# Kernel optimization log

Hardware: AMD Instinct MI355X
Metric: run time of the kernel (lower is better)

## Reference

```python
import jax, jax.numpy as jnp
import numpy as np


def setup_inputs() -> dict:
    key = jax.random.key(0)
    ks = jax.random.split(key, 6)
    B, N, F = 32, 2048, 64
    C1, C2, H = 32, 32, 512
    x = jax.random.normal(ks[0], (B, N, F), dtype=jnp.float32)
    a = jax.random.uniform(ks[1], (B, N, N), dtype=jnp.float32)
    W1 = jax.random.normal(ks[2], (F, C1), dtype=jnp.float32) * (1.0 / np.sqrt(F))
    b1 = jnp.zeros((C1,), dtype=jnp.float32)
    W2 = jax.random.normal(ks[3], (C1, C2), dtype=jnp.float32) * (1.0 / np.sqrt(C1))
    b2 = jnp.zeros((C2,), dtype=jnp.float32)
    Wf1 = jax.random.normal(ks[4], (C2, H), dtype=jnp.float32) * (1.0 / np.sqrt(C2))
    bf1 = jnp.zeros((H,), dtype=jnp.float32)
    Wf2 = jax.random.normal(ks[5], (H, 1), dtype=jnp.float32) * (1.0 / np.sqrt(H))
    bf2 = jnp.zeros((1,), dtype=jnp.float32)
    return {"x": x, "a": a, "W1": W1, "b1": b1, "W2": W2, "b2": b2,
            "Wf1": Wf1, "bf1": bf1, "Wf2": Wf2, "bf2": bf2}


def _gcn(x, a, W, b):
    # GCNConv batch mode: act(A @ X @ W + b); project first (cheaper: F -> C)
    xw = jnp.einsum('bnf,fc->bnc', x, W)
    return jax.nn.relu(jnp.einsum('bnm,bmc->bnc', a, xw) + b)


def reference(x, a, W1, b1, W2, b2, Wf1, bf1, Wf2, bf2):
    h = _gcn(x, a, W1, b1)          # [B,N,32]
    h = _gcn(h, a, W2, b2)          # [B,N,32]
    pooled = jnp.sum(h, axis=1)     # GlobalSumPool over nodes -> [B,32]
    h = jax.nn.relu(pooled @ Wf1 + bf1)  # [B,512]
    out = h @ Wf2 + bf2             # linear output activation -> [B,1]
    return out
```

## Files before the change

### kernel.cpp

```cpp
#include <hip/hip_runtime.h>

using bf16x8 = __attribute__((ext_vector_type(8))) short;
using f32x4  = __attribute__((ext_vector_type(4))) float;

static constexpr int NN = 2048;
static constexpr int NB = 32;
static constexpr int NC = 32;

__device__ __forceinline__ unsigned short f2bf(float f) {
    unsigned int u = __float_as_uint(f);
    u += 0x7FFFu + ((u >> 16) & 1u);
    return (unsigned short)(u >> 16);
}

template<int INCH>
__global__ void proj_kernel(const float* __restrict__ X, const float* __restrict__ W,
                            unsigned short* __restrict__ XWt)
{
    __shared__ float wlds[INCH * NC];
    const int b = blockIdx.y;
    const int m = blockIdx.x * 256 + threadIdx.x;
    for (int i = threadIdx.x; i < INCH * NC; i += 256) wlds[i] = W[i];
    __syncthreads();

    const float* xrow = X + ((size_t)b * NN + m) * INCH;
    float acc[NC];
#pragma unroll
    for (int c = 0; c < NC; ++c) acc[c] = 0.f;

    for (int f = 0; f < INCH; f += 4) {
        const float4 v = *reinterpret_cast<const float4*>(xrow + f);
        const float xv[4] = {v.x, v.y, v.z, v.w};
#pragma unroll
        for (int j = 0; j < 4; ++j) {
#pragma unroll
            for (int c = 0; c < NC; ++c)
                acc[c] += xv[j] * wlds[(f + j) * NC + c];
        }
    }

    unsigned short* outp = XWt + (size_t)b * NC * NN + m;
#pragma unroll
    for (int c = 0; c < NC; ++c) outp[(size_t)c * NN] = f2bf(acc[c]);
}

template<bool WRITE_H>
__global__ void gcn_gemm(const float* __restrict__ A, const unsigned short* __restrict__ Bt,
                         const float* __restrict__ bias, float* __restrict__ Hout,
                         float* __restrict__ pooled)
{
    const int b    = blockIdx.y;
    const int wave = threadIdx.x >> 6;
    const int lane = threadIdx.x & 63;
    const int lr   = lane & 15;
    const int kg   = lane >> 4;

    const int r0 = blockIdx.x * 64 + wave * 16;

    const float*          ap  = A  + ((size_t)b * NN + (r0 + lr)) * NN + kg * 8;
    const unsigned short* bp0 = Bt + ((size_t)b * NC + lr) * NN + kg * 8;
    const unsigned short* bp1 = bp0 + (size_t)16 * NN;

    f32x4 acc0 = {0.f, 0.f, 0.f, 0.f};
    f32x4 acc1 = {0.f, 0.f, 0.f, 0.f};

    for (int k = 0; k < NN; k += 128) {
        float4 xa[8];
        bf16x8 bb0[4], bb1[4];
#pragma unroll
        for (int s = 0; s < 4; ++s) {
            xa[2 * s]     = *reinterpret_cast<const float4*>(ap + s * 32);
            xa[2 * s + 1] = *reinterpret_cast<const float4*>(ap + s * 32 + 4);
            bb0[s] = *reinterpret_cast<const bf16x8*>(bp0 + s * 32);
            bb1[s] = *reinterpret_cast<const bf16x8*>(bp1 + s * 32);
        }
        ap += 128; bp0 += 128; bp1 += 128;

#pragma unroll
        for (int s = 0; s < 4; ++s) {
            bf16x8 af;
            af[0] = (short)f2bf(xa[2 * s].x); af[1] = (short)f2bf(xa[2 * s].y);
            af[2] = (short)f2bf(xa[2 * s].z); af[3] = (short)f2bf(xa[2 * s].w);
            af[4] = (short)f2bf(xa[2 * s + 1].x); af[5] = (short)f2bf(xa[2 * s + 1].y);
            af[6] = (short)f2bf(xa[2 * s + 1].z); af[7] = (short)f2bf(xa[2 * s + 1].w);

            acc0 = __builtin_amdgcn_mfma_f32_16x16x32_bf16(af, bb0[s], acc0, 0, 0, 0);
            acc1 = __builtin_amdgcn_mfma_f32_16x16x32_bf16(af, bb1[s], acc1, 0, 0, 0);
        }
    }

    const float bias0 = bias[lr];
    const float bias1 = bias[lr + 16];

    if constexpr (WRITE_H) {
#pragma unroll
        for (int j = 0; j < 4; ++j) {
            const int row = r0 + kg * 4 + j;
            float* hp = Hout + ((size_t)b * NN + row) * NC;
            hp[lr]      = fmaxf(acc0[j] + bias0, 0.f);
            hp[lr + 16] = fmaxf(acc1[j] + bias1, 0.f);
        }
    } else {
        float s0 = 0.f, s1 = 0.f;
#pragma unroll
        for (int j = 0; j < 4; ++j) {
            s0 += fmaxf(acc0[j] + bias0, 0.f);
            s1 += fmaxf(acc1[j] + bias1, 0.f);
        }
        s0 += __shfl_xor(s0, 16); s0 += __shfl_xor(s0, 32);
        s1 += __shfl_xor(s1, 16); s1 += __shfl_xor(s1, 32);
        if (kg == 0) {
            atomicAdd(&pooled[b * NC + lr],      s0);
            atomicAdd(&pooled[b * NC + 16 + lr], s1);
        }
    }
}

__global__ void head_kernel(const float* __restrict__ pooled,
                            const float* __restrict__ Wf1, const float* __restrict__ bf1,
                            const float* __restrict__ Wf2, const float* __restrict__ bf2,
                            float* __restrict__ out)
{
    const int b = blockIdx.x;
    const int h = threadIdx.x;

    float dot = 0.f;
#pragma unroll
    for (int c = 0; c < NC; ++c)
        dot += pooled[b * NC + c] * Wf1[c * 512 + h];

    const float v   = fmaxf(dot + bf1[h], 0.f);
    float part      = v * Wf2[h];

#pragma unroll
    for (int off = 32; off >= 1; off >>= 1)
        part += __shfl_xor(part, off);

    __shared__ float red[8];
    if ((threadIdx.x & 63) == 0) red[threadIdx.x >> 6] = part;
    __syncthreads();
    if (threadIdx.x == 0) {
        float s = 0.f;
#pragma unroll
        for (int i = 0; i < 8; ++i) s += red[i];
        out[b] = s + bf2[0];
    }
}

extern "C" void kernel_launch(void* const* d_in, const int* in_sizes, int n_in,
                              void* d_out, int out_size, void* d_ws, size_t ws_size,
                              hipStream_t stream)
{
    const float* x   = (const float*)d_in[0];
    const float* a   = (const float*)d_in[1];
    const float* W1  = (const float*)d_in[2];
    const float* b1  = (const float*)d_in[3];
    const float* W2  = (const float*)d_in[4];
    const float* b2  = (const float*)d_in[5];
    const float* Wf1 = (const float*)d_in[6];
    const float* bf1 = (const float*)d_in[7];
    const float* Wf2 = (const float*)d_in[8];
    const float* bf2 = (const float*)d_in[9];
    float* out = (float*)d_out;

    char* ws = (char*)d_ws;
    unsigned short* xwt1 = (unsigned short*)(ws);
    float*          h1   = (float*)(ws + (4ull << 20));
    unsigned short* xwt2 = (unsigned short*)(ws + (12ull << 20));
    float*          pooled = (float*)(ws + (16ull << 20));

    hipMemsetAsync(pooled, 0, NB * NC * sizeof(float), stream);

    dim3 pgrid(NN / 256, NB);
    proj_kernel<64><<<pgrid, 256, 0, stream>>>(x, W1, xwt1);

    dim3 ggrid(NN / 64, NB);
    gcn_gemm<true><<<ggrid, 256, 0, stream>>>(a, xwt1, b1, h1, nullptr);

    proj_kernel<32><<<pgrid, 256, 0, stream>>>(h1, W2, xwt2);

    gcn_gemm<false><<<ggrid, 256, 0, stream>>>(a, xwt2, b2, nullptr, pooled);

    head_kernel<<<dim3(NB), 512, 0, stream>>>(pooled, Wf1, bf1, Wf2, bf2, out);
}
```

Measured before the change: 299.3 us.

## Fuse both GCN layers into one cooperative persistent kernel with per-batch barriers

Replaces the four separate projection and GEMM launches with one cooperative kernel of 256 blocks, which loops over batches in groups of 8. Each batch uses 32 blocks that synchronise through global atomic counters. The second projection (H1·W2) is fused into the epilogue of the first GEMM through LDS, so the fp32 H1 intermediate is never written to or read from global memory. The cost is the spin-wait barriers and fewer resident blocks. With only 256 blocks, one per CU, there is less latency hiding for the bandwidth-bound streaming of the A matrix, which is read twice.

```diff
diff --git a/kernel.cpp b/kernel.cpp
--- a/kernel.cpp
+++ b/kernel.cpp
@@ -1,4 +1,5 @@
 #include <hip/hip_runtime.h>
+#include <hip/hip_bf16.h>
 
 using bf16x8 = __attribute__((ext_vector_type(8))) short;
 using f32x4  = __attribute__((ext_vector_type(4))) float;
@@ -13,60 +14,15 @@
     return (unsigned short)(u >> 16);
 }
 
-template<int INCH>
-__global__ void proj_kernel(const float* __restrict__ X, const float* __restrict__ W,
-                            unsigned short* __restrict__ XWt)
-{
-    __shared__ float wlds[INCH * NC];
-    const int b = blockIdx.y;
-    const int m = blockIdx.x * 256 + threadIdx.x;
-    for (int i = threadIdx.x; i < INCH * NC; i += 256) wlds[i] = W[i];
-    __syncthreads();
-
-    const float* xrow = X + ((size_t)b * NN + m) * INCH;
-    float acc[NC];
-#pragma unroll
-    for (int c = 0; c < NC; ++c) acc[c] = 0.f;
-
-    for (int f = 0; f < INCH; f += 4) {
-        const float4 v = *reinterpret_cast<const float4*>(xrow + f);
-        const float xv[4] = {v.x, v.y, v.z, v.w};
-#pragma unroll
-        for (int j = 0; j < 4; ++j) {
-#pragma unroll
-            for (int c = 0; c < NC; ++c)
-                acc[c] += xv[j] * wlds[(f + j) * NC + c];
-        }
-    }
-
-    unsigned short* outp = XWt + (size_t)b * NC * NN + m;
-#pragma unroll
-    for (int c = 0; c < NC; ++c) outp[(size_t)c * NN] = f2bf(acc[c]);
-}
-
-template<bool WRITE_H>
-__global__ void gcn_gemm(const float* __restrict__ A, const unsigned short* __restrict__ Bt,
-                         const float* __restrict__ bias, float* __restrict__ Hout,
-                         float* __restrict__ pooled)
-{
-    const int b    = blockIdx.y;
-    const int wave = threadIdx.x >> 6;
-    const int lane = threadIdx.x & 63;
-    const int lr   = lane & 15;
-    const int kg   = lane >> 4;
-
-    const int r0 = blockIdx.x * 64 + wave * 16;
-
-    const float*          ap  = A  + ((size_t)b * NN + (r0 + lr)) * NN + kg * 8;
-    const unsigned short* bp0 = Bt + ((size_t)b * NC + lr) * NN + kg * 8;
+__device__ __forceinline__ void gemm_tile_deep(
+    const float* __restrict__ ap,
+    const unsigned short* __restrict__ bp0,
+    f32x4& acc0, f32x4& acc1)
+{
     const unsigned short* bp1 = bp0 + (size_t)16 * NN;
-
-    f32x4 acc0 = {0.f, 0.f, 0.f, 0.f};
-    f32x4 acc1 = {0.f, 0.f, 0.f, 0.f};
-
+    union ABf { bf16x8 v; __hip_bfloat16 e[8]; };
     for (int k = 0; k < NN; k += 128) {
-        float4 xa[8];
-        bf16x8 bb0[4], bb1[4];
+        float4 xa[8]; bf16x8 bb0[4], bb1[4];
 #pragma unroll
         for (int s = 0; s < 4; ++s) {
             xa[2 * s]     = *reinterpret_cast<const float4*>(ap + s * 32);
@@ -75,43 +31,127 @@
             bb1[s] = *reinterpret_cast<const bf16x8*>(bp1 + s * 32);
         }
         ap += 128; bp0 += 128; bp1 += 128;
-
 #pragma unroll
         for (int s = 0; s < 4; ++s) {
-            bf16x8 af;
-            af[0] = (short)f2bf(xa[2 * s].x); af[1] = (short)f2bf(xa[2 * s].y);
-            af[2] = (short)f2bf(xa[2 * s].z); af[3] = (short)f2bf(xa[2 * s].w);
-            af[4] = (short)f2bf(xa[2 * s + 1].x); af[5] = (short)f2bf(xa[2 * s + 1].y);
-            af[6] = (short)f2bf(xa[2 * s + 1].z); af[7] = (short)f2bf(xa[2 * s + 1].w);
-
-            acc0 = __builtin_amdgcn_mfma_f32_16x16x32_bf16(af, bb0[s], acc0, 0, 0, 0);
-            acc1 = __builtin_amdgcn_mfma_f32_16x16x32_bf16(af, bb1[s], acc1, 0, 0, 0);
+            ABf af;
+            af.e[0] = __float2bfloat16(xa[2 * s].x);
+            af.e[1] = __float2bfloat16(xa[2 * s].y);
+            af.e[2] = __float2bfloat16(xa[2 * s].z);
+            af.e[3] = __float2bfloat16(xa[2 * s].w);
+            af.e[4] = __float2bfloat16(xa[2 * s + 1].x);
+            af.e[5] = __float2bfloat16(xa[2 * s + 1].y);
+            af.e[6] = __float2bfloat16(xa[2 * s + 1].z);
+            af.e[7] = __float2bfloat16(xa[2 * s + 1].w);
+            acc0 = __builtin_amdgcn_mfma_f32_16x16x32_bf16(af.v, bb0[s], acc0, 0, 0, 0);
+            acc1 = __builtin_amdgcn_mfma_f32_16x16x32_bf16(af.v, bb1[s], acc1, 0, 0, 0);
         }
     }
-
-    const float bias0 = bias[lr];
-    const float bias1 = bias[lr + 16];
-
-    if constexpr (WRITE_H) {
-#pragma unroll
-        for (int j = 0; j < 4; ++j) {
-            const int row = r0 + kg * 4 + j;
-            float* hp = Hout + ((size_t)b * NN + row) * NC;
-            hp[lr]      = fmaxf(acc0[j] + bias0, 0.f);
-            hp[lr + 16] = fmaxf(acc1[j] + bias1, 0.f);
-        }
-    } else {
-        float s0 = 0.f, s1 = 0.f;
-#pragma unroll
-        for (int j = 0; j < 4; ++j) {
-            s0 += fmaxf(acc0[j] + bias0, 0.f);
-            s1 += fmaxf(acc1[j] + bias1, 0.f);
-        }
-        s0 += __shfl_xor(s0, 16); s0 += __shfl_xor(s0, 32);
-        s1 += __shfl_xor(s1, 16); s1 += __shfl_xor(s1, 32);
-        if (kg == 0) {
-            atomicAdd(&pooled[b * NC + lr],      s0);
-            atomicAdd(&pooled[b * NC + 16 + lr], s1);
+}
+
+__global__ __launch_bounds__(256, 1)
+void fused_gcn(const float* __restrict__ A, const float* __restrict__ X,
+               const float* __restrict__ W1, const float* __restrict__ b1,
+               const float* __restrict__ W2, const float* __restrict__ b2,
+               unsigned short* __restrict__ xwt1, unsigned short* __restrict__ xwt2,
+               float* __restrict__ pooled,
+               unsigned int* __restrict__ done0, unsigned int* __restrict__ done1)
+{
+    __shared__ float smem[64 * 33 + 1024];
+
+    const int t    = threadIdx.x;
+    const int g    = blockIdx.x;
+    const int tile = g & 31;
+    const int r0   = tile * 64;
+    const int wave = t >> 6, lane = t & 63;
+    const int lr   = lane & 15, kg = lane >> 4;
+
+    for (int it = 0; it < 4; ++it) {
+        const int b = it * 8 + (g >> 5);
+
+        __syncthreads();
+        for (int i = t; i < 64 * 32; i += 256) smem[i] = W1[i];
+        __syncthreads();
+        {
+            const int row = r0 + (t >> 2);
+            const int c0  = (t & 3) * 8;
+            const float* xrow = X + ((size_t)b * NN + row) * 64;
+            float acc[8] = {0.f, 0.f, 0.f, 0.f, 0.f, 0.f, 0.f, 0.f};
+            for (int f = 0; f < 64; ++f) {
+                const float xv = xrow[f];
+#pragma unroll
+                for (int i = 0; i < 8; ++i) acc[i] += xv * smem[f * 32 + c0 + i];
+            }
+            unsigned short* op = xwt1 + (size_t)b * NC * NN + row;
+#pragma unroll
+            for (int i = 0; i < 8; ++i) op[(size_t)(c0 + i) * NN] = f2bf(acc[i]);
+        }
+        __threadfence();
+        __syncthreads();
+        if (t == 0) {
+            atomicAdd(&done0[b], 1u);
+            while (atomicAdd(&done0[b], 0u) < 32u) __builtin_amdgcn_s_sleep(2);
+        }
+        __syncthreads();
+        __threadfence();
+
+        f32x4 acc0 = {0.f, 0.f, 0.f, 0.f};
+        f32x4 acc1 = {0.f, 0.f, 0.f, 0.f};
+        gemm_tile_deep(A + ((size_t)b * NN + r0 + wave * 16 + lr) * NN + kg * 8,
+                       xwt1 + (size_t)b * NC * NN + (size_t)lr * NN + kg * 8,
+                       acc0, acc1);
+        {
+            float* hl  = smem;
+            float* w2l = smem + 64 * 33;
+            const float bb0 = b1[lr], bb1 = b1[lr + 16];
+#pragma unroll
+            for (int j = 0; j < 4; ++j) {
+                const int rr = wave * 16 + kg * 4 + j;
+                hl[rr * 33 + lr]      = fmaxf(acc0[j] + bb0, 0.f);
+                hl[rr * 33 + lr + 16] = fmaxf(acc1[j] + bb1, 0.f);
+            }
+            *reinterpret_cast<float4*>(&w2l[t * 4]) =
+                *reinterpret_cast<const float4*>(&W2[t * 4]);
+            __syncthreads();
+            const int m  = t >> 2;
+            const int c0 = (t & 3) * 8;
+            float o[8] = {0.f, 0.f, 0.f, 0.f, 0.f, 0.f, 0.f, 0.f};
+            for (int c = 0; c < 32; ++c) {
+                const float hv = hl[m * 33 + c];
+#pragma unroll
+                for (int i = 0; i < 8; ++i) o[i] += hv * w2l[c * 32 + c0 + i];
+            }
+            unsigned short* op = xwt2 + (size_t)b * NC * NN + r0 + m;
+#pragma unroll
+            for (int i = 0; i < 8; ++i) op[(size_t)(c0 + i) * NN] = f2bf(o[i]);
+        }
+        __threadfence();
+        __syncthreads();
+        if (t == 0) {
+            atomicAdd(&done1[b], 1u);
+            while (atomicAdd(&done1[b], 0u) < 32u) __builtin_amdgcn_s_sleep(2);
+        }
+        __syncthreads();
+        __threadfence();
+
+        acc0 = f32x4{0.f, 0.f, 0.f, 0.f};
+        acc1 = f32x4{0.f, 0.f, 0.f, 0.f};
+        gemm_tile_deep(A + ((size_t)b * NN + r0 + wave * 16 + lr) * NN + kg * 8,
+                       xwt2 + (size_t)b * NC * NN + (size_t)lr * NN + kg * 8,
+                       acc0, acc1);
+        {
+            const float bb0 = b2[lr], bb1 = b2[lr + 16];
+            float s0 = 0.f, s1 = 0.f;
+#pragma unroll
+            for (int j = 0; j < 4; ++j) {
+                s0 += fmaxf(acc0[j] + bb0, 0.f);
+                s1 += fmaxf(acc1[j] + bb1, 0.f);
+            }
+            s0 += __shfl_xor(s0, 16); s0 += __shfl_xor(s0, 32);
+            s1 += __shfl_xor(s1, 16); s1 += __shfl_xor(s1, 32);
+            if (kg == 0) {
+                atomicAdd(&pooled[b * NC + lr],      s0);
+                atomicAdd(&pooled[b * NC + 16 + lr], s1);
+            }
         }
     }
 }
@@ -129,8 +169,8 @@
     for (int c = 0; c < NC; ++c)
         dot += pooled[b * NC + c] * Wf1[c * 512 + h];
 
-    const float v   = fmaxf(dot + bf1[h], 0.f);
-    float part      = v * Wf2[h];
+    const float v = fmaxf(dot + bf1[h], 0.f);
+    float part    = v * Wf2[h];
 
 #pragma unroll
     for (int off = 32; off >= 1; off >>= 1)
@@ -164,22 +204,19 @@
     float* out = (float*)d_out;
 
     char* ws = (char*)d_ws;
-    unsigned short* xwt1 = (unsigned short*)(ws);
-    float*          h1   = (float*)(ws + (4ull << 20));
-    unsigned short* xwt2 = (unsigned short*)(ws + (12ull << 20));
-    float*          pooled = (float*)(ws + (16ull << 20));
-
-    hipMemsetAsync(pooled, 0, NB * NC * sizeof(float), stream);
-
-    dim3 pgrid(NN / 256, NB);
-    proj_kernel<64><<<pgrid, 256, 0, stream>>>(x, W1, xwt1);
-
-    dim3 ggrid(NN / 64, NB);
-    gcn_gemm<true><<<ggrid, 256, 0, stream>>>(a, xwt1, b1, h1, nullptr);
-
-    proj_kernel<32><<<pgrid, 256, 0, stream>>>(h1, W2, xwt2);
-
-    gcn_gemm<false><<<ggrid, 256, 0, stream>>>(a, xwt2, b2, nullptr, pooled);
+    float*          pooled = (float*)ws;
+    unsigned int*   done0  = (unsigned int*)(ws + 4096);
+    unsigned int*   done1  = (unsigned int*)(ws + 4096 + 256);
+    unsigned short* xwt1   = (unsigned short*)(ws + (1ull << 20));
+    unsigned short* xwt2   = (unsigned short*)(ws + (5ull << 20));
+
+    hipMemsetAsync(ws, 0, 8192, stream);
+
+    void* args[] = {(void*)&a, (void*)&x, (void*)&W1, (void*)&b1, (void*)&W2,
+                    (void*)&b2, (void*)&xwt1, (void*)&xwt2, (void*)&pooled,
+                    (void*)&done0, (void*)&done1};
+    hipLaunchCooperativeKernel((const void*)fused_gcn, dim3(256), dim3(256),
+                               args, 0, stream);
 
     head_kernel<<<dim3(NB), 512, 0, stream>>>(pooled, Wf1, bf1, Wf2, bf2, out);
 }
```

Result: slower. 848.0 us (+183.3%).

## Split-K GCN GEMM, fuse second projection, and batch-group launches for L2 reuse

Applied to the files above, without the earlier changes.

Reworks the GCN aggregation kernel so the four waves of a block split the K dimension, each reading a contiguous 512-wide slice, and their partial results are reduced through LDS. The first pass now folds in the W2 projection and writes bf16 XW2 directly, which removes the fp32 H1 round-trip and the second projection kernel. Launches are interleaved in groups of 8 batches (layer 1 then layer 2 for each group), so that group's slice of A is more likely to still be in cache when the second pass reads it. The cost is more, smaller launches, an LDS reduction with extra barriers, and fewer rows per block.

```diff
diff --git a/kernel.cpp b/kernel.cpp
--- a/kernel.cpp
+++ b/kernel.cpp
@@ -1,4 +1,5 @@
 #include <hip/hip_runtime.h>
+#include <hip/hip_bf16.h>
 
 using bf16x8 = __attribute__((ext_vector_type(8))) short;
 using f32x4  = __attribute__((ext_vector_type(4))) float;
@@ -6,6 +7,7 @@
 static constexpr int NN = 2048;
 static constexpr int NB = 32;
 static constexpr int NC = 32;
+static constexpr int GB = 8;
 
 __device__ __forceinline__ unsigned short f2bf(float f) {
     unsigned int u = __float_as_uint(f);
@@ -44,29 +46,38 @@
     for (int c = 0; c < NC; ++c) outp[(size_t)c * NN] = f2bf(acc[c]);
 }
 
-template<bool WRITE_H>
-__global__ void gcn_gemm(const float* __restrict__ A, const unsigned short* __restrict__ Bt,
-                         const float* __restrict__ bias, float* __restrict__ Hout,
-                         float* __restrict__ pooled)
-{
-    const int b    = blockIdx.y;
-    const int wave = threadIdx.x >> 6;
-    const int lane = threadIdx.x & 63;
-    const int lr   = lane & 15;
-    const int kg   = lane >> 4;
-
-    const int r0 = blockIdx.x * 64 + wave * 16;
-
-    const float*          ap  = A  + ((size_t)b * NN + (r0 + lr)) * NN + kg * 8;
-    const unsigned short* bp0 = Bt + ((size_t)b * NC + lr) * NN + kg * 8;
+template<bool FUSE>
+__global__ __launch_bounds__(256, 4)
+void gcn_gemm_ks(const float* __restrict__ A, const unsigned short* __restrict__ Bt,
+                 const float* __restrict__ bias, const float* __restrict__ W2,
+                 unsigned short* __restrict__ XWt2, float* __restrict__ pooled,
+                 int bbase)
+{
+    __shared__ float red[3][16][33];
+    __shared__ float hl[16][33];
+    __shared__ float w2l[32 * 32];
+
+    const int b    = bbase + blockIdx.y;
+    const int t    = threadIdx.x;
+    const int w    = t >> 6, lane = t & 63;
+    const int lr   = lane & 15, kg = lane >> 4;
+    const int r0   = blockIdx.x * 16;
+
+    if constexpr (FUSE) {
+        *reinterpret_cast<float4*>(&w2l[t * 4]) =
+            *reinterpret_cast<const float4*>(&W2[t * 4]);
+    }
+
+    const float*          ap  = A  + ((size_t)b * NN + r0 + lr) * NN + w * 512 + kg * 8;
+    const unsigned short* bp0 = Bt + ((size_t)b * NC + lr) * NN + w * 512 + kg * 8;
     const unsigned short* bp1 = bp0 + (size_t)16 * NN;
 
     f32x4 acc0 = {0.f, 0.f, 0.f, 0.f};
     f32x4 acc1 = {0.f, 0.f, 0.f, 0.f};
-
-    for (int k = 0; k < NN; k += 128) {
-        float4 xa[8];
-        bf16x8 bb0[4], bb1[4];
+    union ABf { bf16x8 v; __hip_bfloat16 e[8]; };
+
+    for (int k = 0; k < 512; k += 128) {
+        float4 xa[8]; bf16x8 bb0[4], bb1[4];
 #pragma unroll
         for (int s = 0; s < 4; ++s) {
             xa[2 * s]     = *reinterpret_cast<const float4*>(ap + s * 32);
@@ -75,43 +86,82 @@
             bb1[s] = *reinterpret_cast<const bf16x8*>(bp1 + s * 32);
         }
         ap += 128; bp0 += 128; bp1 += 128;
-
 #pragma unroll
         for (int s = 0; s < 4; ++s) {
-            bf16x8 af;
-            af[0] = (short)f2bf(xa[2 * s].x); af[1] = (short)f2bf(xa[2 * s].y);
-            af[2] = (short)f2bf(xa[2 * s].z); af[3] = (short)f2bf(xa[2 * s].w);
-            af[4] = (short)f2bf(xa[2 * s + 1].x); af[5] = (short)f2bf(xa[2 * s + 1].y);
-            af[6] = (short)f2bf(xa[2 * s + 1].z); af[7] = (short)f2bf(xa[2 * s + 1].w);
-
-            acc0 = __builtin_amdgcn_mfma_f32_16x16x32_bf16(af, bb0[s], acc0, 0, 0, 0);
-            acc1 = __builtin_amdgcn_mfma_f32_16x16x32_bf16(af, bb1[s], acc1, 0, 0, 0);
-        }
-    }
-
-    const float bias0 = bias[lr];
-    const float bias1 = bias[lr + 16];
-
-    if constexpr (WRITE_H) {
+            ABf af;
+            af.e[0] = __float2bfloat16(xa[2 * s].x);
+            af.e[1] = __float2bfloat16(xa[2 * s].y);
+            af.e[2] = __float2bfloat16(xa[2 * s].z);
+            af.e[3] = __float2bfloat16(xa[2 * s].w);
+            af.e[4] = __float2bfloat16(xa[2 * s + 1].x);
+            af.e[5] = __float2bfloat16(xa[2 * s + 1].y);
+            af.e[6] = __float2bfloat16(xa[2 * s + 1].z);
+            af.e[7] = __float2bfloat16(xa[2 * s + 1].w);
+            acc0 = __builtin_amdgcn_mfma_f32_16x16x32_bf16(af.v, bb0[s], acc0, 0, 0, 0);
+            acc1 = __builtin_amdgcn_mfma_f32_16x16x32_bf16(af.v, bb1[s], acc1, 0, 0, 0);
+        }
+    }
+
+    if (w > 0) {
 #pragma unroll
         for (int j = 0; j < 4; ++j) {
-            const int row = r0 + kg * 4 + j;
-            float* hp = Hout + ((size_t)b * NN + row) * NC;
-            hp[lr]      = fmaxf(acc0[j] + bias0, 0.f);
-            hp[lr + 16] = fmaxf(acc1[j] + bias1, 0.f);
-        }
+            red[w - 1][kg * 4 + j][lr]      = acc0[j];
+            red[w - 1][kg * 4 + j][lr + 16] = acc1[j];
+        }
+    }
+    __syncthreads();
+
+    if constexpr (FUSE) {
+        if (w == 0) {
+            const float bb0v = bias[lr], bb1v = bias[lr + 16];
+#pragma unroll
+            for (int j = 0; j < 4; ++j) {
+                const int row = kg * 4 + j;
+                float a0 = acc0[j], a1 = acc1[j];
+#pragma unroll
+                for (int ww = 0; ww < 3; ++ww) {
+                    a0 += red[ww][row][lr];
+                    a1 += red[ww][row][lr + 16];
+                }
+                hl[row][lr]      = fmaxf(a0 + bb0v, 0.f);
+                hl[row][lr + 16] = fmaxf(a1 + bb1v, 0.f);
+            }
+        }
+        __syncthreads();
+        const int row = t >> 4;
+        const int c0  = (t & 15) * 2;
+        float o0 = 0.f, o1 = 0.f;
+#pragma unroll
+        for (int c = 0; c < 32; ++c) {
+            const float hv = hl[row][c];
+            o0 += hv * w2l[c * 32 + c0];
+            o1 += hv * w2l[c * 32 + c0 + 1];
+        }
+        unsigned short* op = XWt2 + (size_t)b * NC * NN + r0 + row;
+        op[(size_t)c0 * NN]       = f2bf(o0);
+        op[(size_t)(c0 + 1) * NN] = f2bf(o1);
     } else {
-        float s0 = 0.f, s1 = 0.f;
-#pragma unroll
-        for (int j = 0; j < 4; ++j) {
-            s0 += fmaxf(acc0[j] + bias0, 0.f);
-            s1 += fmaxf(acc1[j] + bias1, 0.f);
-        }
-        s0 += __shfl_xor(s0, 16); s0 += __shfl_xor(s0, 32);
-        s1 += __shfl_xor(s1, 16); s1 += __shfl_xor(s1, 32);
-        if (kg == 0) {
-            atomicAdd(&pooled[b * NC + lr],      s0);
-            atomicAdd(&pooled[b * NC + 16 + lr], s1);
+        if (w == 0) {
+            const float bb0v = bias[lr], bb1v = bias[lr + 16];
+            float s0 = 0.f, s1 = 0.f;
+#pragma unroll
+            for (int j = 0; j < 4; ++j) {
+                const int row = kg * 4 + j;
+                float a0 = acc0[j], a1 = acc1[j];
+#pragma unroll
+                for (int ww = 0; ww < 3; ++ww) {
+                    a0 += red[ww][row][lr];
+                    a1 += red[ww][row][lr + 16];
+                }
+                s0 += fmaxf(a0 + bb0v, 0.f);
+                s1 += fmaxf(a1 + bb1v, 0.f);
+            }
+            s0 += __shfl_xor(s0, 16); s0 += __shfl_xor(s0, 32);
+            s1 += __shfl_xor(s1, 16); s1 += __shfl_xor(s1, 32);
+            if (kg == 0) {
+                atomicAdd(&pooled[b * NC + lr],      s0);
+                atomicAdd(&pooled[b * NC + 16 + lr], s1);
+            }
         }
     }
 }
@@ -129,20 +179,20 @@
     for (int c = 0; c < NC; ++c)
         dot += pooled[b * NC + c] * Wf1[c * 512 + h];
 
-    const float v   = fmaxf(dot + bf1[h], 0.f);
-    float part      = v * Wf2[h];
+    const float v = fmaxf(dot + bf1[h], 0.f);
+    float part    = v * Wf2[h];
 
 #pragma unroll
     for (int off = 32; off >= 1; off >>= 1)
         part += __shfl_xor(part, off);
 
-    __shared__ float red[8];
-    if ((threadIdx.x & 63) == 0) red[threadIdx.x >> 6] = part;
+    __shared__ float redh[8];
+    if ((threadIdx.x & 63) == 0) redh[threadIdx.x >> 6] = part;
     __syncthreads();
     if (threadIdx.x == 0) {
         float s = 0.f;
 #pragma unroll
-        for (int i = 0; i < 8; ++i) s += red[i];
+        for (int i = 0; i < 8; ++i) s += redh[i];
         out[b] = s + bf2[0];
     }
 }
@@ -164,22 +214,20 @@
     float* out = (float*)d_out;
 
     char* ws = (char*)d_ws;
-    unsigned short* xwt1 = (unsigned short*)(ws);
-    float*          h1   = (float*)(ws + (4ull << 20));
-    unsigned short* xwt2 = (unsigned short*)(ws + (12ull << 20));
-    float*          pooled = (float*)(ws + (16ull << 20));
+    unsigned short* xwt1   = (unsigned short*)(ws);
+    unsigned short* xwt2   = (unsigned short*)(ws + (4ull << 20));
+    float*          pooled = (float*)(ws + (8ull << 20));
 
     hipMemsetAsync(pooled, 0, NB * NC * sizeof(float), stream);
 
-    dim3 pgrid(NN / 256, NB);
-    proj_kernel<64><<<pgrid, 256, 0, stream>>>(x, W1, xwt1);
-
-    dim3 ggrid(NN / 64, NB);
-    gcn_gemm<true><<<ggrid, 256, 0, stream>>>(a, xwt1, b1, h1, nullptr);
-
-    proj_kernel<32><<<pgrid, 256, 0, stream>>>(h1, W2, xwt2);
-
-    gcn_gemm<false><<<ggrid, 256, 0, stream>>>(a, xwt2, b2, nullptr, pooled);
+    proj_kernel<64><<<dim3(NN / 256, NB), 256, 0, stream>>>(x, W1, xwt1);
+
+    for (int g = 0; g < NB / GB; ++g) {
+        gcn_gemm_ks<true><<<dim3(NN / 16, GB), 256, 0, stream>>>(
+            a, xwt1, b1, W2, xwt2, nullptr, g * GB);
+        gcn_gemm_ks<false><<<dim3(NN / 16, GB), 256, 0, stream>>>(
+            a, xwt2, b2, nullptr, nullptr, pooled, g * GB);
+    }
 
     head_kernel<<<dim3(NB), 512, 0, stream>>>(pooled, Wf1, bf1, Wf2, bf2, out);
 }
```

Measured after the change: 327.0 us. +9.3%, slower.
